# Kernel tuning notes

Hardware: AMD Instinct MI355X
Metric: run time of the kernel (lower is better)

Reference implementation:

```python
import jax, jax.numpy as jnp
import numpy as np

B = 4096      # batch
F = 16        # num fields
V = 20000     # field vocab size
E = 64        # embed size
HID = 1024    # hidden width (all hidden layers equal, required by the reshape trick)
NODE_IN = F * E  # 1024
NL = 3        # number of hidden layers stacked into attention (len(layer_sizes)-2)


def _xavier(key, shape):
    fan_in, fan_out = shape[0], shape[1]
    lim = np.sqrt(6.0 / (fan_in + fan_out)).astype(np.float32)
    return jax.random.uniform(key, shape, jnp.float32, -lim, lim)


def setup_inputs() -> dict:
    key = jax.random.key(0)
    ks = jax.random.split(key, 8)
    idx = jax.random.randint(ks[0], (B, F), 0, V)
    emb = _xavier(ks[1], (V, E))  # share init shape, then tile per-field via fold_in
    emb = jnp.stack([_xavier(jax.random.fold_in(ks[1], f), (V, E)) for f in range(F)], axis=0)  # [F,V,E]
    w0 = _xavier(ks[2], (NODE_IN, HID)); b0 = jnp.zeros((HID,), jnp.float32)
    w1 = _xavier(ks[3], (HID, HID));     b1 = jnp.zeros((HID,), jnp.float32)
    w2 = _xavier(ks[4], (HID, HID));     b2 = jnp.zeros((HID,), jnp.float32)
    w3 = _xavier(ks[5], (HID, HID));     b3 = jnp.zeros((HID,), jnp.float32)
    w_final = _xavier(ks[6], (2 * HID, 1)); b_final = jnp.zeros((1,), jnp.float32)
    return {"idx": idx, "emb": emb, "w0": w0, "b0": b0, "w1": w1, "b1": b1,
            "w2": w2, "b2": b2, "w3": w3, "b3": b3,
            "w_final": w_final, "b_final": b_final}


def reference(idx, emb, w0, b0, w1, b1, w2, b2, w3, b3, w_final, b_final):
    bsz = idx.shape[0]
    # sparse one-hot @ embed == gather: [B,F,E] -> [B, F*E]
    xw = emb[jnp.arange(F)[None, :], idx].reshape(bsz, F * E)
    # MLP stack (dropout in test mode: keep_prob=1, i.e. identity)
    l0 = jax.nn.relu(xw @ w0 + b0)
    l1 = jax.nn.relu(l0 @ w1 + b1)
    l2 = jax.nn.relu(l1 @ w2 + b2)
    l_final = jax.nn.relu(l2 @ w3 + b3)
    # faithful reproduction of tf.concat(axis=0) then reshape([-1, NL, HID])
    cat = jnp.concatenate([l0, l1, l2], axis=0)          # [NL*B, HID]
    Hm = cat.reshape(bsz, NL, HID)                        # H[b,j] = cat[NL*b + j]
    mask = 1.0 - jnp.eye(NL, dtype=Hm.dtype)              # zero diagonal
    S = jnp.einsum('bih,bjh->bij', Hm, Hm) * mask         # [B, NL, NL]
    A = jax.nn.softmax(S, axis=-1)                        # attention over layers
    G = jnp.einsum('bij,bjh->bh', A, Hm)                  # reduce_sum(A@H, axis=1)
    M = jnp.concatenate([l_final, G], axis=1)             # [B, 2*HID]
    out = (M @ w_final + b_final).squeeze(-1)             # logits [B]
    return out
```

## Files before the change

kernel.cpp:

```cpp
#include <hip/hip_runtime.h>
#include <hip/hip_bf16.h>
#include <stdint.h>

#define B_SZ 4096
#define F_N 16
#define V_SZ 20000
#define E_SZ 64
#define HID 1024

typedef __attribute__((ext_vector_type(8))) _Float16 f16x8;
typedef __attribute__((ext_vector_type(4))) _Float16 f16x4;
typedef __attribute__((ext_vector_type(4))) float f32x4;

__device__ __forceinline__ void gload16(const void* g, void* l) {
  __builtin_amdgcn_global_load_lds(
      (const __attribute__((address_space(1))) void*)g,
      (__attribute__((address_space(3))) void*)l, 16, 0, 0);
}

__device__ __forceinline__ int s3(int r) { return (r ^ (r >> 3)) & 7; }

__global__ __launch_bounds__(256) void prep(
    const int* __restrict__ idx, const float* __restrict__ emb,
    const float* __restrict__ w0, const float* __restrict__ w1,
    const float* __restrict__ w2, const float* __restrict__ w3,
    _Float16* __restrict__ wt, _Float16* __restrict__ xw) {
  const int cb = blockIdx.x;
  if (cb < 4096) {
    const int z = cb >> 10, rem = cb & 1023;
    const float* w = (z == 0) ? w0 : (z == 1) ? w1 : (z == 2) ? w2 : w3;
    _Float16* outp = wt + (size_t)z * HID * HID;
    __shared__ float tile[32][33];
    const int tx = threadIdx.x & 31, ty = threadIdx.x >> 5;
    const int k0 = (rem >> 5) * 32, n0 = (rem & 31) * 32;
#pragma unroll
    for (int q = 0; q < 4; ++q) {
      int r = ty + q * 8;
      tile[r][tx] = w[(size_t)(k0 + r) * HID + n0 + tx];
    }
    __syncthreads();
#pragma unroll
    for (int q = 0; q < 4; ++q) {
      int r = ty + q * 8;
      outp[(size_t)(n0 + r) * HID + k0 + tx] = (_Float16)tile[tx][r];
    }
  } else {
    int i = (cb - 4096) * 256 + threadIdx.x;
    int b = i >> 8;
    int r = i & 255;
    int f = r >> 4;
    int e4 = r & 15;
    int id = idx[b * F_N + f];
    float4 v = *(const float4*)(emb + ((size_t)f * V_SZ + id) * E_SZ + e4 * 4);
    f16x4 h = {(_Float16)v.x, (_Float16)v.y, (_Float16)v.z, (_Float16)v.w};
    *(f16x4*)(xw + (size_t)b * HID + r * 4) = h;
  }
}

__global__ __launch_bounds__(512) void gemm_mfma(
    const _Float16* __restrict__ A, const _Float16* __restrict__ Wt,
    const float* __restrict__ bias, _Float16* __restrict__ C) {
  __shared__ _Float16 As[2][128 * 64];
  __shared__ _Float16 Bs[2][128 * 64];

  const int t = threadIdx.x;
  const int l = ((blockIdx.x & 7) << 5) | (blockIdx.x >> 3);
  const int bm = (l >> 3) * 128, bn = (l & 7) * 128;

  const int w = t >> 6, lane = t & 63;
  const int wr = w >> 2, wc = w & 3;
  const int lr = lane & 15, lg = lane >> 4;

  const int srow = t >> 3;
  const int cdst = t & 7;
  const int csrc = cdst ^ s3(srow);
  const _Float16* ga0 = A + (size_t)(bm + srow) * HID + csrc * 8;
  const _Float16* gb0 = Wt + (size_t)(bn + srow) * HID + csrc * 8;
  const int ld0 = t * 8, ld1 = t * 8 + 4096;

  int aoff[4], boff[2];
#pragma unroll
  for (int mi = 0; mi < 4; mi++) {
    int ra = wr * 64 + mi * 16 + lr;
    aoff[mi] = ra * 64 + ((lg ^ s3(ra)) * 8);
  }
#pragma unroll
  for (int ni = 0; ni < 2; ni++) {
    int rb = wc * 32 + ni * 16 + lr;
    boff[ni] = rb * 64 + ((lg ^ s3(rb)) * 8);
  }

  f32x4 acc[4][2] = {};

#define STAGE(buf, ko)                              \
  gload16(ga0 + (ko), &As[buf][ld0]);               \
  gload16(ga0 + (ko) + 64 * HID, &As[buf][ld1]);    \
  gload16(gb0 + (ko), &Bs[buf][ld0]);               \
  gload16(gb0 + (ko) + 64 * HID, &Bs[buf][ld1]);

  STAGE(0, 0)

  for (int tI = 0; tI < 16; ++tI) {
    const int cur = tI & 1;
    if (tI < 15) {
      STAGE(cur ^ 1, (tI + 1) * 64)
    }
    if (tI < 15)
      asm volatile("s_waitcnt vmcnt(4)" ::: "memory");
    else
      asm volatile("s_waitcnt vmcnt(0)" ::: "memory");
    asm volatile("s_barrier" ::: "memory");

    f16x8 a0[4], a1[4], b0[2], b1[2];
#pragma unroll
    for (int mi = 0; mi < 4; mi++) {
      a0[mi] = *(const f16x8*)&As[cur][aoff[mi]];
      a1[mi] = *(const f16x8*)&As[cur][aoff[mi] ^ 32];
    }
#pragma unroll
    for (int ni = 0; ni < 2; ni++) {
      b0[ni] = *(const f16x8*)&Bs[cur][boff[ni]];
      b1[ni] = *(const f16x8*)&Bs[cur][boff[ni] ^ 32];
    }
#pragma unroll
    for (int mi = 0; mi < 4; mi++)
#pragma unroll
      for (int ni = 0; ni < 2; ni++) {
        acc[mi][ni] = __builtin_amdgcn_mfma_f32_16x16x32_f16(
            a0[mi], b0[ni], acc[mi][ni], 0, 0, 0);
        acc[mi][ni] = __builtin_amdgcn_mfma_f32_16x16x32_f16(
            a1[mi], b1[ni], acc[mi][ni], 0, 0, 0);
      }

    asm volatile("s_barrier" ::: "memory");
  }
#undef STAGE

#pragma unroll
  for (int ni = 0; ni < 2; ni++) {
    int col = bn + wc * 32 + ni * 16 + lr;
    float bv = bias[col];
#pragma unroll
    for (int mi = 0; mi < 4; mi++) {
      int rbase = bm + wr * 64 + mi * 16 + lg * 4;
#pragma unroll
      for (int j = 0; j < 4; j++) {
        float x = acc[mi][ni][j] + bv;
        x = x > 0.f ? x : 0.f;
        C[(size_t)(rbase + j) * HID + col] = (_Float16)x;
      }
    }
  }
}

__global__ __launch_bounds__(256) void attn_final(
    const _Float16* __restrict__ cat, const _Float16* __restrict__ lf,
    const float* __restrict__ wf, const float* __restrict__ bfin,
    float* __restrict__ out) {
  const int wave = threadIdx.x >> 6;
  const int lane = threadIdx.x & 63;
  const int b = blockIdx.x * 4 + wave;

  const _Float16* h0 = cat + (size_t)(3 * b + 0) * 1024;
  const _Float16* h1 = cat + (size_t)(3 * b + 1) * 1024;
  const _Float16* h2 = cat + (size_t)(3 * b + 2) * 1024;
  const _Float16* lfr = lf + (size_t)b * 1024;

  float s01 = 0.f, s02 = 0.f, s12 = 0.f;
  float d0 = 0.f, d1 = 0.f, d2 = 0.f, dl = 0.f;

#pragma unroll
  for (int q = 0; q < 2; ++q) {
    int e8 = (lane + q * 64) * 8;
    f16x8 a0 = *(const f16x8*)(h0 + e8);
    f16x8 a1 = *(const f16x8*)(h1 + e8);
    f16x8 a2 = *(const f16x8*)(h2 + e8);
    f16x8 al = *(const f16x8*)(lfr + e8);
    float4 u0a = *(const float4*)(wf + e8);
    float4 u0b = *(const float4*)(wf + e8 + 4);
    float4 u1a = *(const float4*)(wf + 1024 + e8);
    float4 u1b = *(const float4*)(wf + 1024 + e8 + 4);
    float wf0[8] = {u0a.x, u0a.y, u0a.z, u0a.w, u0b.x, u0b.y, u0b.z, u0b.w};
    float wf1[8] = {u1a.x, u1a.y, u1a.z, u1a.w, u1b.x, u1b.y, u1b.z, u1b.w};
#pragma unroll
    for (int j = 0; j < 8; ++j) {
      float p0 = (float)a0[j], p1 = (float)a1[j], p2 = (float)a2[j];
      float pl = (float)al[j];
      s01 = fmaf(p0, p1, s01);
      s02 = fmaf(p0, p2, s02);
      s12 = fmaf(p1, p2, s12);
      d0 = fmaf(p0, wf1[j], d0);
      d1 = fmaf(p1, wf1[j], d1);
      d2 = fmaf(p2, wf1[j], d2);
      dl = fmaf(pl, wf0[j], dl);
    }
  }

#pragma unroll
  for (int m = 1; m < 64; m <<= 1) {
    s01 += __shfl_xor(s01, m);
    s02 += __shfl_xor(s02, m);
    s12 += __shfl_xor(s12, m);
    d0 += __shfl_xor(d0, m);
    d1 += __shfl_xor(d1, m);
    d2 += __shfl_xor(d2, m);
    dl += __shfl_xor(dl, m);
  }

  if (lane == 0) {
    float c0 = 0.f, c1 = 0.f, c2 = 0.f;
    {
      float m = fmaxf(0.f, fmaxf(s01, s02));
      float e0 = expf(0.f - m), e1 = expf(s01 - m), e2 = expf(s02 - m);
      float inv = 1.f / (e0 + e1 + e2);
      c0 += e0 * inv; c1 += e1 * inv; c2 += e2 * inv;
    }
    {
      float m = fmaxf(s01, fmaxf(0.f, s12));
      float e0 = expf(s01 - m), e1 = expf(0.f - m), e2 = expf(s12 - m);
      float inv = 1.f / (e0 + e1 + e2);
      c0 += e0 * inv; c1 += e1 * inv; c2 += e2 * inv;
    }
    {
      float m = fmaxf(s02, fmaxf(s12, 0.f));
      float e0 = expf(s02 - m), e1 = expf(s12 - m), e2 = expf(0.f - m);
      float inv = 1.f / (e0 + e1 + e2);
      c0 += e0 * inv; c1 += e1 * inv; c2 += e2 * inv;
    }
    out[b] = dl + c0 * d0 + c1 * d1 + c2 * d2 + bfin[0];
  }
}

extern "C" void kernel_launch(void* const* d_in, const int* in_sizes, int n_in,
                              void* d_out, int out_size, void* d_ws,
                              size_t ws_size, hipStream_t stream) {
  const int* idx = (const int*)d_in[0];
  const float* emb = (const float*)d_in[1];
  const float* w0 = (const float*)d_in[2];
  const float* b0 = (const float*)d_in[3];
  const float* w1 = (const float*)d_in[4];
  const float* b1 = (const float*)d_in[5];
  const float* w2 = (const float*)d_in[6];
  const float* b2 = (const float*)d_in[7];
  const float* w3 = (const float*)d_in[8];
  const float* b3 = (const float*)d_in[9];
  const float* wf = (const float*)d_in[10];
  const float* bfin = (const float*)d_in[11];
  float* out = (float*)d_out;

  const size_t RB = (size_t)B_SZ * HID;
  const size_t WSZ = (size_t)HID * HID;

  _Float16* wt = (_Float16*)d_ws;
  _Float16* xw16 = wt + 4 * WSZ;
  _Float16* cat16 = xw16 + RB;
  _Float16* lf16 = cat16 + 3 * RB;

  prep<<<8192, 256, 0, stream>>>(idx, emb, w0, w1, w2, w3, wt, xw16);

  gemm_mfma<<<256, 512, 0, stream>>>(xw16, wt + 0 * WSZ, b0, cat16);
  gemm_mfma<<<256, 512, 0, stream>>>(cat16, wt + 1 * WSZ, b1, cat16 + RB);
  gemm_mfma<<<256, 512, 0, stream>>>(cat16 + RB, wt + 2 * WSZ, b2,
                                     cat16 + 2 * RB);
  gemm_mfma<<<256, 512, 0, stream>>>(cat16 + 2 * RB, wt + 3 * WSZ, b3, lf16);

  attn_final<<<B_SZ / 4, 256, 0, stream>>>(cat16, lf16, wf, bfin, out);
}
```

Before: 80.90 us.

## Load GEMM B operand directly into registers and triple-buffer A tiles

The MFMA GEMM no longer stages the weight (B) tile through shared memory. Each wave loads its B fragments from global memory straight into registers, double-buffered across k-steps. The A tile moves to a three-buffer LDS ring with manual vmcnt waits, and s_setprio is raised around the MFMA block. The weight-transpose prep kernel switches to 64x32 tiles that write packed 32-bit half pairs. The aim is to cut LDS traffic and barrier stalls, at the cost of redundant global/L2 reads of B across waves and more fragile wait counting.

```diff
diff --git a/kernel.cpp b/kernel.cpp
--- a/kernel.cpp
+++ b/kernel.cpp
@@ -26,26 +26,34 @@
     const float* __restrict__ w2, const float* __restrict__ w3,
     _Float16* __restrict__ wt, _Float16* __restrict__ xw) {
   const int cb = blockIdx.x;
-  if (cb < 4096) {
-    const int z = cb >> 10, rem = cb & 1023;
+  const int t = threadIdx.x;
+  if (cb < 2048) {
+    const int z = cb >> 9, rem = cb & 511;
     const float* w = (z == 0) ? w0 : (z == 1) ? w1 : (z == 2) ? w2 : w3;
     _Float16* outp = wt + (size_t)z * HID * HID;
-    __shared__ float tile[32][33];
-    const int tx = threadIdx.x & 31, ty = threadIdx.x >> 5;
-    const int k0 = (rem >> 5) * 32, n0 = (rem & 31) * 32;
+    __shared__ float tile[64][33];
+    const int k0 = (rem >> 5) * 64, n0 = (rem & 31) * 32;
+    const int c = t & 31;
+#pragma unroll
+    for (int q = 0; q < 8; ++q) {
+      int r = (t >> 5) + q * 8;
+      tile[r][c] = w[(size_t)(k0 + r) * HID + n0 + c];
+    }
+    __syncthreads();
 #pragma unroll
     for (int q = 0; q < 4; ++q) {
-      int r = ty + q * 8;
-      tile[r][tx] = w[(size_t)(k0 + r) * HID + n0 + tx];
-    }
-    __syncthreads();
-#pragma unroll
-    for (int q = 0; q < 4; ++q) {
-      int r = ty + q * 8;
-      outp[(size_t)(n0 + r) * HID + k0 + tx] = (_Float16)tile[tx][r];
+      int s = t + q * 256;
+      int n = s >> 5, c2 = s & 31;
+      f16x4 dummy;  (void)dummy;
+      __hip_bfloat16* unused = nullptr; (void)unused;
+      _Float16 lo = (_Float16)tile[2 * c2][n];
+      _Float16 hi = (_Float16)tile[2 * c2 + 1][n];
+      union { _Float16 h[2]; uint32_t u; } p;
+      p.h[0] = lo; p.h[1] = hi;
+      *(uint32_t*)(outp + (size_t)(n0 + n) * HID + k0 + 2 * c2) = p.u;
     }
   } else {
-    int i = (cb - 4096) * 256 + threadIdx.x;
+    int i = (cb - 2048) * 256 + t;
     int b = i >> 8;
     int r = i & 255;
     int f = r >> 4;
@@ -60,8 +68,7 @@
 __global__ __launch_bounds__(512) void gemm_mfma(
     const _Float16* __restrict__ A, const _Float16* __restrict__ Wt,
     const float* __restrict__ bias, _Float16* __restrict__ C) {
-  __shared__ _Float16 As[2][128 * 64];
-  __shared__ _Float16 Bs[2][128 * 64];
+  __shared__ _Float16 As[3][128 * 64];
 
   const int t = threadIdx.x;
   const int l = ((blockIdx.x & 7) << 5) | (blockIdx.x >> 3);
@@ -71,69 +78,90 @@
   const int wr = w >> 2, wc = w & 3;
   const int lr = lane & 15, lg = lane >> 4;
 
-  const int srow = t >> 3;
-  const int cdst = t & 7;
+  const int srow = t >> 3, cdst = t & 7;
   const int csrc = cdst ^ s3(srow);
   const _Float16* ga0 = A + (size_t)(bm + srow) * HID + csrc * 8;
-  const _Float16* gb0 = Wt + (size_t)(bn + srow) * HID + csrc * 8;
   const int ld0 = t * 8, ld1 = t * 8 + 4096;
 
-  int aoff[4], boff[2];
+#define STAGE(buf, ko)                                  \
+  gload16(ga0 + (ko), &As[buf][ld0]);                   \
+  gload16(ga0 + (ko) + (size_t)64 * HID, &As[buf][ld1]);
+
+  int aoff[4];
 #pragma unroll
   for (int mi = 0; mi < 4; mi++) {
     int ra = wr * 64 + mi * 16 + lr;
     aoff[mi] = ra * 64 + ((lg ^ s3(ra)) * 8);
   }
-#pragma unroll
-  for (int ni = 0; ni < 2; ni++) {
-    int rb = wc * 32 + ni * 16 + lr;
-    boff[ni] = rb * 64 + ((lg ^ s3(rb)) * 8);
-  }
+
+  const _Float16* gB0 = Wt + (size_t)(bn + wc * 32 + lr) * HID + lg * 8;
+  const _Float16* gB1 = gB0 + (size_t)16 * HID;
 
   f32x4 acc[4][2] = {};
-
-#define STAGE(buf, ko)                              \
-  gload16(ga0 + (ko), &As[buf][ld0]);               \
-  gload16(ga0 + (ko) + 64 * HID, &As[buf][ld1]);    \
-  gload16(gb0 + (ko), &Bs[buf][ld0]);               \
-  gload16(gb0 + (ko) + 64 * HID, &Bs[buf][ld1]);
+  f16x8 bE[2][2], bO[2][2];
 
   STAGE(0, 0)
-
-  for (int tI = 0; tI < 16; ++tI) {
-    const int cur = tI & 1;
-    if (tI < 15) {
-      STAGE(cur ^ 1, (tI + 1) * 64)
-    }
-    if (tI < 15)
-      asm volatile("s_waitcnt vmcnt(4)" ::: "memory");
+#pragma unroll
+  for (int kk = 0; kk < 2; kk++) {
+    bE[0][kk] = *(const f16x8*)(gB0 + kk * 32);
+    bE[1][kk] = *(const f16x8*)(gB1 + kk * 32);
+  }
+  STAGE(1, 64)
+
+#define COMPUTE(BUF, BREG)                                                   \
+  {                                                                          \
+    f16x8 a0[4], a1[4];                                                      \
+    _Pragma("unroll") for (int mi = 0; mi < 4; mi++) {                       \
+      a0[mi] = *(const f16x8*)&As[BUF][aoff[mi]];                            \
+      a1[mi] = *(const f16x8*)&As[BUF][aoff[mi] ^ 32];                       \
+    }                                                                        \
+    __builtin_amdgcn_s_setprio(1);                                           \
+    _Pragma("unroll") for (int mi = 0; mi < 4; mi++)                         \
+        _Pragma("unroll") for (int ni = 0; ni < 2; ni++) {                   \
+      acc[mi][ni] = __builtin_amdgcn_mfma_f32_16x16x32_f16(                  \
+          a0[mi], BREG[ni][0], acc[mi][ni], 0, 0, 0);                        \
+      acc[mi][ni] = __builtin_amdgcn_mfma_f32_16x16x32_f16(                  \
+          a1[mi], BREG[ni][1], acc[mi][ni], 0, 0, 0);                        \
+    }                                                                        \
+    __builtin_amdgcn_s_setprio(0);                                           \
+  }
+
+#pragma unroll
+  for (int u = 0; u < 8; ++u) {
+    const int ta = 2 * u, tb = 2 * u + 1;
+    asm volatile("s_waitcnt vmcnt(2)" ::: "memory");
+    asm volatile("s_barrier" ::: "memory");
+    {
+      const int kn = (ta + 1) * 64;
+#pragma unroll
+      for (int kk = 0; kk < 2; kk++) {
+        bO[0][kk] = *(const f16x8*)(gB0 + kn + kk * 32);
+        bO[1][kk] = *(const f16x8*)(gB1 + kn + kk * 32);
+      }
+    }
+    if (ta + 2 < 16) {
+      STAGE((ta + 2) % 3, (ta + 2) * 64)
+    }
+    COMPUTE(ta % 3, bE)
+    if (tb == 15)
+      asm volatile("s_waitcnt vmcnt(0)" ::: "memory");
     else
-      asm volatile("s_waitcnt vmcnt(0)" ::: "memory");
+      asm volatile("s_waitcnt vmcnt(2)" ::: "memory");
     asm volatile("s_barrier" ::: "memory");
-
-    f16x8 a0[4], a1[4], b0[2], b1[2];
-#pragma unroll
-    for (int mi = 0; mi < 4; mi++) {
-      a0[mi] = *(const f16x8*)&As[cur][aoff[mi]];
-      a1[mi] = *(const f16x8*)&As[cur][aoff[mi] ^ 32];
-    }
-#pragma unroll
-    for (int ni = 0; ni < 2; ni++) {
-      b0[ni] = *(const f16x8*)&Bs[cur][boff[ni]];
-      b1[ni] = *(const f16x8*)&Bs[cur][boff[ni] ^ 32];
-    }
-#pragma unroll
-    for (int mi = 0; mi < 4; mi++)
-#pragma unroll
-      for (int ni = 0; ni < 2; ni++) {
-        acc[mi][ni] = __builtin_amdgcn_mfma_f32_16x16x32_f16(
-            a0[mi], b0[ni], acc[mi][ni], 0, 0, 0);
-        acc[mi][ni] = __builtin_amdgcn_mfma_f32_16x16x32_f16(
-            a1[mi], b1[ni], acc[mi][ni], 0, 0, 0);
+    if (tb + 1 < 16) {
+      const int kn = (tb + 1) * 64;
+#pragma unroll
+      for (int kk = 0; kk < 2; kk++) {
+        bE[0][kk] = *(const f16x8*)(gB0 + kn + kk * 32);
+        bE[1][kk] = *(const f16x8*)(gB1 + kn + kk * 32);
       }
-
-    asm volatile("s_barrier" ::: "memory");
-  }
+    }
+    if (tb + 2 < 16) {
+      STAGE((tb + 2) % 3, (tb + 2) * 64)
+    }
+    COMPUTE(tb % 3, bO)
+  }
+#undef COMPUTE
 #undef STAGE
 
 #pragma unroll
@@ -256,7 +284,7 @@
   _Float16* cat16 = xw16 + RB;
   _Float16* lf16 = cat16 + 3 * RB;
 
-  prep<<<8192, 256, 0, stream>>>(idx, emb, w0, w1, w2, w3, wt, xw16);
+  prep<<<6144, 256, 0, stream>>>(idx, emb, w0, w1, w2, w3, wt, xw16);
 
   gemm_mfma<<<256, 512, 0, stream>>>(xw16, wt + 0 * WSZ, b0, cat16);
   gemm_mfma<<<256, 512, 0, stream>>>(cat16, wt + 1 * WSZ, b1, cat16 + RB);
```

Measured after the change: 119.5 us. +47.7%, slower.

## Split K across wave pairs in GEMM with LDS reduction; widen transpose stores

Applied to the files above, without the earlier changes.

The GEMM now assigns each wave a 64x64 output tile over half of each 64-wide K slice, with wave pairs splitting K. The partial sums are combined through LDS at the end before bias and ReLU. This cuts LDS fragment reads per MFMA, since each wave reuses 4 A and 4 B fragments across 16 MFMAs instead of 4 and 2 across 8 pairs. The cost is a larger accumulator register footprint and an extra reduction and barrier. The weight transpose in prep also moves to 64x32 tiles with packed 32-bit fp16 stores and fewer blocks.

```diff
diff --git a/kernel.cpp b/kernel.cpp
--- a/kernel.cpp
+++ b/kernel.cpp
@@ -26,26 +26,32 @@
     const float* __restrict__ w2, const float* __restrict__ w3,
     _Float16* __restrict__ wt, _Float16* __restrict__ xw) {
   const int cb = blockIdx.x;
-  if (cb < 4096) {
-    const int z = cb >> 10, rem = cb & 1023;
+  const int t = threadIdx.x;
+  if (cb < 2048) {
+    const int z = cb >> 9, rem = cb & 511;
     const float* w = (z == 0) ? w0 : (z == 1) ? w1 : (z == 2) ? w2 : w3;
     _Float16* outp = wt + (size_t)z * HID * HID;
-    __shared__ float tile[32][33];
-    const int tx = threadIdx.x & 31, ty = threadIdx.x >> 5;
-    const int k0 = (rem >> 5) * 32, n0 = (rem & 31) * 32;
+    __shared__ float tile[64][33];
+    const int k0 = (rem >> 5) * 64, n0 = (rem & 31) * 32;
+    const int c = t & 31;
+#pragma unroll
+    for (int q = 0; q < 8; ++q) {
+      int r = (t >> 5) + q * 8;
+      tile[r][c] = w[(size_t)(k0 + r) * HID + n0 + c];
+    }
+    __syncthreads();
 #pragma unroll
     for (int q = 0; q < 4; ++q) {
-      int r = ty + q * 8;
-      tile[r][tx] = w[(size_t)(k0 + r) * HID + n0 + tx];
-    }
-    __syncthreads();
-#pragma unroll
-    for (int q = 0; q < 4; ++q) {
-      int r = ty + q * 8;
-      outp[(size_t)(n0 + r) * HID + k0 + tx] = (_Float16)tile[tx][r];
+      int s = t + q * 256;
+      int n = s >> 5, c2 = s & 31;
+      _Float16 lo = (_Float16)tile[2 * c2][n];
+      _Float16 hi = (_Float16)tile[2 * c2 + 1][n];
+      union { _Float16 h[2]; uint32_t u; } p;
+      p.h[0] = lo; p.h[1] = hi;
+      *(uint32_t*)(outp + (size_t)(n0 + n) * HID + k0 + 2 * c2) = p.u;
     }
   } else {
-    int i = (cb - 4096) * 256 + threadIdx.x;
+    int i = (cb - 2048) * 256 + t;
     int b = i >> 8;
     int r = i & 255;
     int f = r >> 4;
@@ -60,43 +66,40 @@
 __global__ __launch_bounds__(512) void gemm_mfma(
     const _Float16* __restrict__ A, const _Float16* __restrict__ Wt,
     const float* __restrict__ bias, _Float16* __restrict__ C) {
-  __shared__ _Float16 As[2][128 * 64];
-  __shared__ _Float16 Bs[2][128 * 64];
+  __shared__ __align__(16) _Float16 sh[2][2][128 * 64];
+#define AS(b) (sh[b][0])
+#define BS(b) (sh[b][1])
 
   const int t = threadIdx.x;
   const int l = ((blockIdx.x & 7) << 5) | (blockIdx.x >> 3);
   const int bm = (l >> 3) * 128, bn = (l & 7) * 128;
 
   const int w = t >> 6, lane = t & 63;
-  const int wr = w >> 2, wc = w & 3;
+  const int wk = w & 1, wn = (w >> 1) & 1, wm = w >> 2;
   const int lr = lane & 15, lg = lane >> 4;
 
-  const int srow = t >> 3;
-  const int cdst = t & 7;
+  const int srow = t >> 3, cdst = t & 7;
   const int csrc = cdst ^ s3(srow);
   const _Float16* ga0 = A + (size_t)(bm + srow) * HID + csrc * 8;
   const _Float16* gb0 = Wt + (size_t)(bn + srow) * HID + csrc * 8;
   const int ld0 = t * 8, ld1 = t * 8 + 4096;
 
-  int aoff[4], boff[2];
-#pragma unroll
-  for (int mi = 0; mi < 4; mi++) {
-    int ra = wr * 64 + mi * 16 + lr;
-    aoff[mi] = ra * 64 + ((lg ^ s3(ra)) * 8);
-  }
-#pragma unroll
-  for (int ni = 0; ni < 2; ni++) {
-    int rb = wc * 32 + ni * 16 + lr;
-    boff[ni] = rb * 64 + ((lg ^ s3(rb)) * 8);
-  }
-
-  f32x4 acc[4][2] = {};
-
-#define STAGE(buf, ko)                              \
-  gload16(ga0 + (ko), &As[buf][ld0]);               \
-  gload16(ga0 + (ko) + 64 * HID, &As[buf][ld1]);    \
-  gload16(gb0 + (ko), &Bs[buf][ld0]);               \
-  gload16(gb0 + (ko) + 64 * HID, &Bs[buf][ld1]);
+  int aoff[4], boff[4];
+#pragma unroll
+  for (int i = 0; i < 4; i++) {
+    int ra = wm * 64 + i * 16 + lr;
+    aoff[i] = ra * 64 + (((wk * 4 + lg) ^ s3(ra)) * 8);
+    int rb = wn * 64 + i * 16 + lr;
+    boff[i] = rb * 64 + (((wk * 4 + lg) ^ s3(rb)) * 8);
+  }
+
+  f32x4 acc[4][4] = {};
+
+#define STAGE(buf, ko)                                   \
+  gload16(ga0 + (ko), &AS(buf)[ld0]);                    \
+  gload16(ga0 + (ko) + (size_t)64 * HID, &AS(buf)[ld1]); \
+  gload16(gb0 + (ko), &BS(buf)[ld0]);                    \
+  gload16(gb0 + (ko) + (size_t)64 * HID, &BS(buf)[ld1]);
 
   STAGE(0, 0)
 
@@ -111,46 +114,63 @@
       asm volatile("s_waitcnt vmcnt(0)" ::: "memory");
     asm volatile("s_barrier" ::: "memory");
 
-    f16x8 a0[4], a1[4], b0[2], b1[2];
-#pragma unroll
-    for (int mi = 0; mi < 4; mi++) {
-      a0[mi] = *(const f16x8*)&As[cur][aoff[mi]];
-      a1[mi] = *(const f16x8*)&As[cur][aoff[mi] ^ 32];
-    }
-#pragma unroll
-    for (int ni = 0; ni < 2; ni++) {
-      b0[ni] = *(const f16x8*)&Bs[cur][boff[ni]];
-      b1[ni] = *(const f16x8*)&Bs[cur][boff[ni] ^ 32];
-    }
+    f16x8 a[4], b[4];
+#pragma unroll
+    for (int mi = 0; mi < 4; mi++) a[mi] = *(const f16x8*)&AS(cur)[aoff[mi]];
+#pragma unroll
+    for (int ni = 0; ni < 4; ni++) b[ni] = *(const f16x8*)&BS(cur)[boff[ni]];
 #pragma unroll
     for (int mi = 0; mi < 4; mi++)
 #pragma unroll
-      for (int ni = 0; ni < 2; ni++) {
+      for (int ni = 0; ni < 4; ni++)
         acc[mi][ni] = __builtin_amdgcn_mfma_f32_16x16x32_f16(
-            a0[mi], b0[ni], acc[mi][ni], 0, 0, 0);
-        acc[mi][ni] = __builtin_amdgcn_mfma_f32_16x16x32_f16(
-            a1[mi], b1[ni], acc[mi][ni], 0, 0, 0);
+            a[mi], b[ni], acc[mi][ni], 0, 0, 0);
+
+    asm volatile("s_barrier" ::: "memory");
+  }
+#undef STAGE
+
+  float* red = (float*)&sh[0][0][0];
+  float* R = red + ((wm << 1) | wn) * 4096;
+  if (wk == 1) {
+#pragma unroll
+    for (int mi = 0; mi < 4; mi++)
+#pragma unroll
+      for (int ni = 0; ni < 4; ni++) {
+        int col = ni * 16 + lr;
+        int rb = mi * 4 + lg;
+        *(f32x4*)&R[col * 64 + ((rb ^ (col & 15)) << 2)] = acc[mi][ni];
       }
-
-    asm volatile("s_barrier" ::: "memory");
-  }
-#undef STAGE
-
-#pragma unroll
-  for (int ni = 0; ni < 2; ni++) {
-    int col = bn + wc * 32 + ni * 16 + lr;
-    float bv = bias[col];
-#pragma unroll
-    for (int mi = 0; mi < 4; mi++) {
-      int rbase = bm + wr * 64 + mi * 16 + lg * 4;
-#pragma unroll
-      for (int j = 0; j < 4; j++) {
-        float x = acc[mi][ni][j] + bv;
-        x = x > 0.f ? x : 0.f;
-        C[(size_t)(rbase + j) * HID + col] = (_Float16)x;
+  }
+  asm volatile("s_barrier" ::: "memory");
+  if (wk == 0) {
+#pragma unroll
+    for (int mi = 0; mi < 4; mi++)
+#pragma unroll
+      for (int ni = 0; ni < 4; ni++) {
+        int col = ni * 16 + lr;
+        int rb = mi * 4 + lg;
+        f32x4 p = *(const f32x4*)&R[col * 64 + ((rb ^ (col & 15)) << 2)];
+        acc[mi][ni] += p;
       }
-    }
-  }
+#pragma unroll
+    for (int ni = 0; ni < 4; ni++) {
+      int col = bn + wn * 64 + ni * 16 + lr;
+      float bv = bias[col];
+#pragma unroll
+      for (int mi = 0; mi < 4; mi++) {
+        int rbase = bm + wm * 64 + mi * 16 + lg * 4;
+#pragma unroll
+        for (int j = 0; j < 4; j++) {
+          float x = acc[mi][ni][j] + bv;
+          x = x > 0.f ? x : 0.f;
+          C[(size_t)(rbase + j) * HID + col] = (_Float16)x;
+        }
+      }
+    }
+  }
+#undef AS
+#undef BS
 }
 
 __global__ __launch_bounds__(256) void attn_final(
@@ -256,7 +276,7 @@
   _Float16* cat16 = xw16 + RB;
   _Float16* lf16 = cat16 + 3 * RB;
 
-  prep<<<8192, 256, 0, stream>>>(idx, emb, w0, w1, w2, w3, wt, xw16);
+  prep<<<6144, 256, 0, stream>>>(idx, emb, w0, w1, w2, w3, wt, xw16);
 
   gemm_mfma<<<256, 512, 0, stream>>>(xw16, wt + 0 * WSZ, b0, cat16);
   gemm_mfma<<<256, 512, 0, stream>>>(cat16, wt + 1 * WSZ, b1, cat16 + RB);
```

Result: faster. 73.23 us (-9.5%).
